# Performance work log

Hardware: AMD Instinct MI355X
Metric: run time of the kernel (lower is better)

## Reference

```python
import jax, jax.numpy as jnp
import numpy as np

N = 30000
E = 480000
F_IN = 100
HID = 64
HEADS = 4
NCLS = 47
HC = HEADS * HID  # 256
NEG_SLOPE = 0.2
BN_EPS = 1e-5


def setup_inputs() -> dict:
    key = jax.random.key(0)
    ks = jax.random.split(key, 32)
    s = 0.1
    inp = {
        'x': jax.random.normal(ks[0], (N, F_IN), jnp.float32),
        'edge_index': jax.random.randint(ks[1], (2, E), 0, N, jnp.int32),
        # layer 0: GATConv(F_IN -> HID, heads, concat=True)
        'w0': jax.random.normal(ks[2], (F_IN, HC), jnp.float32) * s,
        'as0': jax.random.normal(ks[3], (HEADS, HID), jnp.float32) * s,
        'ad0': jax.random.normal(ks[4], (HEADS, HID), jnp.float32) * s,
        'b0': jnp.zeros((HC,), jnp.float32),
        'sw0': jax.random.normal(ks[5], (F_IN, HC), jnp.float32) * s,
        'sb0': jnp.zeros((HC,), jnp.float32),
        'g0': jnp.ones((HC,), jnp.float32),
        'be0': jnp.zeros((HC,), jnp.float32),
        # layer 1: GATConv(HC -> HID, heads, concat=True)
        'w1': jax.random.normal(ks[6], (HC, HC), jnp.float32) * s,
        'as1': jax.random.normal(ks[7], (HEADS, HID), jnp.float32) * s,
        'ad1': jax.random.normal(ks[8], (HEADS, HID), jnp.float32) * s,
        'b1': jnp.zeros((HC,), jnp.float32),
        'sw1': jax.random.normal(ks[9], (HC, HC), jnp.float32) * s,
        'sb1': jnp.zeros((HC,), jnp.float32),
        'g1': jnp.ones((HC,), jnp.float32),
        'be1': jnp.zeros((HC,), jnp.float32),
        # layer 2: GATConv(HC -> NCLS, heads, concat=False)
        'w2': jax.random.normal(ks[10], (HC, HEADS * NCLS), jnp.float32) * s,
        'as2': jax.random.normal(ks[11], (HEADS, NCLS), jnp.float32) * s,
        'ad2': jax.random.normal(ks[12], (HEADS, NCLS), jnp.float32) * s,
        'b2': jnp.zeros((NCLS,), jnp.float32),
        'sw2': jax.random.normal(ks[13], (HC, NCLS), jnp.float32) * s,
        'sb2': jnp.zeros((NCLS,), jnp.float32),
    }
    return inp


def gat_conv(x, src, dst, W, a_src, a_dst, bias, heads, out_ch, concat):
    # shared linear for src/dst (PyG GATConv with int in_channels)
    h = (x @ W).reshape(N, heads, out_ch)           # [N,H,C]
    al_s = jnp.sum(h * a_src, axis=-1)              # [N,H]
    al_d = jnp.sum(h * a_dst, axis=-1)              # [N,H]
    e = jax.nn.leaky_relu(al_s[src] + al_d[dst], NEG_SLOPE)  # [E,H]
    # segment (per-destination) softmax
    m = jax.ops.segment_max(e, dst, num_segments=N)
    e = jnp.exp(e - m[dst])
    den = jax.ops.segment_sum(e, dst, num_segments=N)
    alpha = e / (den[dst] + 1e-16)                  # [E,H]
    msg = h[src] * alpha[:, :, None]                # [E,H,C]
    out = jax.ops.segment_sum(msg, dst, num_segments=N)  # [N,H,C]
    out = out.reshape(N, heads * out_ch) if concat else out.mean(axis=1)
    return out + bias


def batch_norm(x, gamma, beta):
    mu = jnp.mean(x, axis=0)
    var = jnp.var(x, axis=0)
    return gamma * (x - mu) * jax.lax.rsqrt(var + BN_EPS) + beta


def reference(x, edge_index, w0, as0, ad0, b0, sw0, sb0, g0, be0,
              w1, as1, ad1, b1, sw1, sb1, g1, be1,
              w2, as2, ad2, b2, sw2, sb2):
    src, dst = edge_index[0], edge_index[1]
    # layer 0
    h = gat_conv(x, src, dst, w0, as0, ad0, b0, HEADS, HID, True)
    h = h + x @ sw0 + sb0
    h = jax.nn.elu(batch_norm(h, g0, be0))
    # layer 1
    h2 = gat_conv(h, src, dst, w1, as1, ad1, b1, HEADS, HID, True)
    h2 = h2 + h @ sw1 + sb1
    h2 = jax.nn.elu(batch_norm(h2, g1, be1))
    # layer 2 (concat=False -> mean over heads)
    out = gat_conv(h2, src, dst, w2, as2, ad2, b2, HEADS, NCLS, False)
    out = out + h2 @ sw2 + sb2
    return jax.nn.log_softmax(out, axis=-1)
```

## Files before the change

kernel.cpp:

```cpp
#include <hip/hip_runtime.h>
#include <math.h>

#define NN 30000
#define EE 480000
#define FIN 100
#define NCLS 47
#define SCAN_B 118

typedef unsigned short ushortt;
typedef __attribute__((ext_vector_type(8))) short bf16x8;
typedef __attribute__((ext_vector_type(4))) float f32x4;
typedef __attribute__((ext_vector_type(2))) float f32x2;

__device__ unsigned char g_H8[(size_t)NN * 256];
__device__ ushortt g_Sb[(size_t)NN * 256];
__device__ float   g_S2[(size_t)NN * 48];
__device__ ushortt g_Fb[(size_t)NN * 256];
__device__ ushortt g_Xb[(size_t)NN * 128];
__device__ ushortt g_Wc0[512 * 128];
__device__ ushortt g_Wc1[512 * 256];
__device__ ushortt g_Wc2[235 * 256];
__device__ float g_als[NN * 4];
__device__ float g_ald[NN * 4];
__device__ int   g_rowptr[NN + 1];
__device__ int   g_counts[NN];
__device__ int   g_bsum[128];
__device__ int   g_esrc[EE];
__device__ float g_stat[1024];

__device__ __forceinline__ float wsum(float v) {
#pragma unroll
  for (int o = 32; o > 0; o >>= 1) v += __shfl_xor(v, o, 64);
  return v;
}
__device__ __forceinline__ float lrelu(float x) { return x > 0.f ? x : 0.2f * x; }
__device__ __forceinline__ ushortt f2bf(float f) {
  unsigned int u = __float_as_uint(f);
  unsigned int r = u + 0x7FFF + ((u >> 16) & 1);
  return (ushortt)(r >> 16);
}
__device__ __forceinline__ float bf2f(ushortt u) {
  return __uint_as_float(((unsigned int)u) << 16);
}
__device__ __forceinline__ unsigned int pk4_fp8(float f0, float f1, float f2, float f3) {
  unsigned int r = 0;
  r = __builtin_amdgcn_cvt_pk_fp8_f32(f0, f1, r, false);
  r = __builtin_amdgcn_cvt_pk_fp8_f32(f2, f3, r, true);
  return r;
}
__device__ __forceinline__ int swz(int row, int k) {
  return (k & ~63) | ((((k >> 3) & 7) ^ (row & 7)) << 3) | (k & 7);
}
__device__ __forceinline__ void glds16(const ushortt* gp, ushortt* lp) {
  __builtin_amdgcn_global_load_lds(
      (const __attribute__((address_space(1))) unsigned int*)gp,
      (__attribute__((address_space(3))) unsigned int*)lp, 16, 0, 0);
}

__global__ void count_kernel(const int* __restrict__ dst) {
  int e = blockIdx.x * blockDim.x + threadIdx.x;
  if (e < EE) atomicAdd(&g_counts[dst[e]], 1);
}
__global__ void scan1_kernel() {
  int i = blockIdx.x * 256 + threadIdx.x;
  int v = (i < NN) ? g_counts[i] : 0;
  __shared__ int sh[4];
  float fv = (float)v;
  fv = wsum(fv);
  if ((threadIdx.x & 63) == 0) sh[threadIdx.x >> 6] = (int)fv;
  __syncthreads();
  if (threadIdx.x == 0) g_bsum[blockIdx.x] = sh[0] + sh[1] + sh[2] + sh[3];
}
__global__ void scan2_kernel() {
  __shared__ int sh[128];
  int t = threadIdx.x;
  int v = (t < SCAN_B) ? g_bsum[t] : 0;
  sh[t] = v;
  __syncthreads();
  for (int off = 1; off < 128; off <<= 1) {
    int x = (t >= off) ? sh[t - off] : 0;
    __syncthreads();
    sh[t] += x;
    __syncthreads();
  }
  g_bsum[t] = sh[t] - v;
}
__global__ void scan3_kernel() {
  __shared__ int sh[256];
  int t = threadIdx.x;
  int i = blockIdx.x * 256 + t;
  int v = (i < NN) ? g_counts[i] : 0;
  sh[t] = v;
  __syncthreads();
  for (int off = 1; off < 256; off <<= 1) {
    int x = (t >= off) ? sh[t - off] : 0;
    __syncthreads();
    sh[t] += x;
    __syncthreads();
  }
  if (i < NN) {
    g_rowptr[i] = g_bsum[blockIdx.x] + sh[t] - v;
    g_counts[i] = 0;
  }
  if (i == NN - 1) g_rowptr[NN] = EE;
}
__global__ void scatter_kernel(const int* __restrict__ dst, const int* __restrict__ src) {
  int e = blockIdx.x * blockDim.x + threadIdx.x;
  if (e < EE) {
    int d = dst[e];
    int pos = g_rowptr[d] + atomicAdd(&g_counts[d], 1);
    g_esrc[pos] = src[e];
  }
}

#define CW0 (512 * 128)
#define CW1 (512 * 256)
#define CW2 (235 * 256)
__global__ void conv_kernel(const float* __restrict__ w0, const float* __restrict__ sw0,
                            const float* __restrict__ w1, const float* __restrict__ sw1,
                            const float* __restrict__ w2, const float* __restrict__ sw2,
                            const float* __restrict__ x) {
  int i = blockIdx.x * blockDim.x + threadIdx.x;
  if (i < CW0) {
    int m = i >> 7, k = i & 127;
    float v = 0.f;
    if (k < FIN) v = (m < 256) ? w0[k * 256 + m] : sw0[k * 256 + (m - 256)];
    g_Wc0[(m << 7) | swz(m, k)] = f2bf(v);
    return;
  }
  i -= CW0;
  if (i < CW1) {
    int m = i >> 8, k = i & 255;
    float v = (m < 256) ? w1[k * 256 + m] : sw1[k * 256 + (m - 256)];
    g_Wc1[(m << 8) | swz(m, k)] = f2bf(v);
    return;
  }
  i -= CW1;
  if (i < CW2) {
    int m = i >> 8, k = i & 255;
    float v = (m < 188) ? w2[(size_t)k * 188 + m] : sw2[(size_t)k * 47 + (m - 188)];
    g_Wc2[(m << 8) | swz(m, k)] = f2bf(v);
    return;
  }
  i -= CW2;
  if (i < NN * 128) {
    int r = i >> 7, k = i & 127;
    g_Xb[(r << 7) | swz(r, k)] = (k < FIN) ? f2bf(x[r * FIN + k]) : 0;
    return;
  }
  i -= NN * 128;
  if (i < NN) {
    g_counts[i] = 0;
    return;
  }
  i -= NN;
  if (i < 1024) g_stat[i] = 0.f;
}

__global__ __launch_bounds__(256) void mfma_gemm(
    const ushortt* __restrict__ A, const ushortt* __restrict__ Wt,
    unsigned char* __restrict__ out8, ushortt* __restrict__ out2b,
    float* __restrict__ out2f,
    int nrows, int Kp, int M, int S, int ld8, int ld2,
    const float* __restrict__ bias2, int pad47,
    const float* __restrict__ a_s, const float* __restrict__ a_d,
    float* __restrict__ alsp, float* __restrict__ aldp) {
  __shared__ __align__(16) ushortt smem[16896];
  ushortt* As = smem;
  ushortt* Ws = smem + 64 * 64;
  float* Ls = (float*)smem;
  int t = threadIdx.x;
  int wave = t >> 6, lane = t & 63;
  int row0 = blockIdx.y * 64, col0 = blockIdx.x * 128;
  int wr = wave >> 1, wc = wave & 1;
  int m16 = lane & 15, q = lane >> 4;
  int rin8 = lane >> 3;
  int koff = (lane & 7) * 8;

  f32x4 acc[2][4];
#pragma unroll
  for (int i = 0; i < 2; i++)
#pragma unroll
    for (int j = 0; j < 4; j++) acc[i][j] = (f32x4){0.f, 0.f, 0.f, 0.f};

  for (int k0 = 0; k0 < Kp; k0 += 64) {
#pragma unroll
    for (int r = 0; r < 2; r++) {
      int lrow = wave * 16 + r * 8;
      int ga = min(row0 + lrow + rin8, nrows - 1);
      glds16(A + (size_t)ga * Kp + k0 + koff, &As[lrow * 64]);
    }
#pragma unroll
    for (int r = 0; r < 4; r++) {
      int lrow = wave * 32 + r * 8;
      int gw = min(col0 + lrow + rin8, M - 1);
      glds16(Wt + (size_t)gw * Kp + k0 + koff, &Ws[lrow * 64]);
    }
    __syncthreads();
#pragma unroll
    for (int c = 0; c < 2; c++) {
      bf16x8 af[2], bf[4];
#pragma unroll
      for (int i = 0; i < 2; i++) {
        int row = wr * 32 + i * 16 + m16;
        int ch = (c * 4 + q) ^ (row & 7);
        af[i] = *(const bf16x8*)(&As[row * 64 + ch * 8]);
      }
#pragma unroll
      for (int i = 0; i < 4; i++) {
        int row = wc * 64 + i * 16 + m16;
        int ch = (c * 4 + q) ^ (row & 7);
        bf[i] = *(const bf16x8*)(&Ws[row * 64 + ch * 8]);
      }
#pragma unroll
      for (int rt = 0; rt < 2; rt++)
#pragma unroll
        for (int ct = 0; ct < 4; ct++)
          acc[rt][ct] = __builtin_amdgcn_mfma_f32_16x16x32_bf16(af[rt], bf[ct], acc[rt][ct], 0, 0, 0);
    }
    __syncthreads();
  }

#pragma unroll
  for (int rt = 0; rt < 2; rt++) {
#pragma unroll
    for (int ctt = 0; ctt < 4; ctt++) {
#pragma unroll
      for (int reg = 0; reg < 4; reg++) {
        int rloc = wr * 32 + rt * 16 + q * 4 + reg;
        Ls[rloc * 132 + wc * 64 + ctt * 16 + m16] = acc[rt][ctt][reg];
      }
    }
  }
  __syncthreads();
  bool all1 = (!pad47) && (col0 + 128 <= S);
  bool all2 = (col0 >= S);
  int row8 = t >> 3, seg = t & 7;
#pragma unroll
  for (int rr = 0; rr < 2; rr++) {
    int rloc = rr * 32 + row8;
    int grow = row0 + rloc;
    if (grow < nrows) {
      const float* lrow = Ls + rloc * 132 + seg * 16;
      int cbase = col0 + seg * 16;
      if (all1) {
        unsigned int q8[4];
#pragma unroll
        for (int kk = 0; kk < 4; kk++)
          q8[kk] = pk4_fp8(lrow[kk * 4], lrow[kk * 4 + 1], lrow[kk * 4 + 2], lrow[kk * 4 + 3]);
        uint4 v8 = {q8[0], q8[1], q8[2], q8[3]};
        *(uint4*)(out8 + (size_t)grow * ld8 + cbase) = v8;
        float s_p = 0.f, d_p = 0.f;
#pragma unroll
        for (int kk = 0; kk < 16; kk++) {
          s_p += lrow[kk] * a_s[cbase + kk];
          d_p += lrow[kk] * a_d[cbase + kk];
        }
        s_p += __shfl_xor(s_p, 1, 64); s_p += __shfl_xor(s_p, 2, 64);
        d_p += __shfl_xor(d_p, 1, 64); d_p += __shfl_xor(d_p, 2, 64);
        if ((seg & 3) == 0) {
          int head = cbase >> 6;
          alsp[grow * 4 + head] = s_p;
          aldp[grow * 4 + head] = d_p;
        }
      } else if (all2) {
        const float* brow = bias2 + (cbase - S);
        ushortt* orow = out2b + (size_t)grow * ld2 + (cbase - S);
        unsigned int pk[8];
#pragma unroll
        for (int kk = 0; kk < 8; kk++) {
          unsigned int lo = f2bf(lrow[kk * 2] + brow[kk * 2]);
          unsigned int hi = f2bf(lrow[kk * 2 + 1] + brow[kk * 2 + 1]);
          pk[kk] = lo | (hi << 16);
        }
        uint4 v0 = {pk[0], pk[1], pk[2], pk[3]};
        uint4 v1 = {pk[4], pk[5], pk[6], pk[7]};
        *(uint4*)(orow) = v0;
        *(uint4*)(orow + 8) = v1;
      } else {
        float pa0 = 0.f, pa1 = 0.f, pd0 = 0.f, pd1 = 0.f;
        int h0 = cbase / 47;
        for (int kk = 0; kk < 16; kk++) {
          int c = cbase + kk;
          if (c >= M) break;
          float v = lrow[kk];
          if (c < S) {
            int hd = c / 47, ch = c - hd * 47;
            int c1 = hd * 48 + ch;
            out8[(size_t)grow * ld8 + c1] =
                (unsigned char)(pk4_fp8(v, 0.f, 0.f, 0.f) & 0xFF);
            if (ch == 46) out8[(size_t)grow * ld8 + c1 + 1] = 0;
            float sw = a_s[hd * 47 + ch], dw = a_d[hd * 47 + ch];
            if (hd == h0) { pa0 += v * sw; pd0 += v * dw; }
            else { pa1 += v * sw; pd1 += v * dw; }
          } else {
            out2f[(size_t)grow * ld2 + (c - S)] = v + bias2[c - S];
          }
        }
        if (pad47 && cbase < S) {
          if (pa0 != 0.f || pd0 != 0.f) {
            atomicAdd(&alsp[grow * 4 + h0], pa0);
            atomicAdd(&aldp[grow * 4 + h0], pd0);
          }
          if ((pa1 != 0.f || pd1 != 0.f) && h0 + 1 < 4) {
            atomicAdd(&alsp[grow * 4 + h0 + 1], pa1);
            atomicAdd(&aldp[grow * 4 + h0 + 1], pd1);
          }
        }
      }
    }
  }
}

__global__ __launch_bounds__(64) void attn_kernel(const unsigned char* __restrict__ H8,
                                                  const float* __restrict__ bias,
                                                  ushortt* __restrict__ Sb) {
  __shared__ __align__(16) float p_sh[64 * 4];
  __shared__ int s_sh[64];
  int n = blockIdx.x, lane = threadIdx.x;
  int rs = g_rowptr[n], deg = g_rowptr[n + 1] - rs;
  float4 ald = *(const float4*)(g_ald + n * 4);
  int q = lane >> 4;
  float den0 = 0, den1 = 0, den2 = 0, den3 = 0;
  float a0 = 0, a1 = 0, a2 = 0, a3 = 0;
  for (int base = 0; base < deg; base += 64) {
    int j = base + lane;
    float p0 = 0, p1 = 0, p2 = 0, p3 = 0;
    int s = 0;
    if (j < deg) {
      s = g_esrc[rs + j];
      float4 av = *(const float4*)(g_als + s * 4);
      p0 = __expf(lrelu(av.x + ald.x)); den0 += p0;
      p1 = __expf(lrelu(av.y + ald.y)); den1 += p1;
      p2 = __expf(lrelu(av.z + ald.z)); den2 += p2;
      p3 = __expf(lrelu(av.w + ald.w)); den3 += p3;
    }
    p_sh[lane * 4 + 0] = p0; p_sh[lane * 4 + 1] = p1;
    p_sh[lane * 4 + 2] = p2; p_sh[lane * 4 + 3] = p3;
    s_sh[lane] = s;
    __syncthreads();
    int cnt = min(64, deg - base);
    for (int jj = 0; jj < cnt; jj++) {
      int ss = s_sh[jj];
      float p = p_sh[jj * 4 + q];
      unsigned int hv = *(const unsigned int*)(H8 + (size_t)ss * 256 + 4 * lane);
      f32x2 lo = __builtin_amdgcn_cvt_pk_f32_fp8(hv, false);
      f32x2 hi = __builtin_amdgcn_cvt_pk_f32_fp8(hv, true);
      a0 += p * lo.x;
      a1 += p * lo.y;
      a2 += p * hi.x;
      a3 += p * hi.y;
    }
    __syncthreads();
  }
  den0 = wsum(den0); den1 = wsum(den1); den2 = wsum(den2); den3 = wsum(den3);
  float denq = (q == 0) ? den0 : (q == 1) ? den1 : (q == 2) ? den2 : den3;
  float inv = 1.f / (denq + 1e-16f);
  size_t o = (size_t)n * 256 + 4 * lane;
  ushort4 sv = *(const ushort4*)(Sb + o);
  float4 bv = *(const float4*)(bias + 4 * lane);
  ushort4 ov;
  ov.x = f2bf(a0 * inv + bv.x + bf2f(sv.x));
  ov.y = f2bf(a1 * inv + bv.y + bf2f(sv.y));
  ov.z = f2bf(a2 * inv + bv.z + bf2f(sv.z));
  ov.w = f2bf(a3 * inv + bv.w + bf2f(sv.w));
  *(ushort4*)(Sb + o) = ov;
}

__global__ __launch_bounds__(64) void attn2_kernel(const unsigned char* __restrict__ H8,
                                                   const float* __restrict__ bias,
                                                   const float* __restrict__ S2,
                                                   float* __restrict__ out) {
  __shared__ __align__(16) float p_sh[64 * 4];
  __shared__ int s_sh[64];
  __shared__ float xh[4][48];
  int n = blockIdx.x, lane = threadIdx.x;
  int rs = g_rowptr[n], deg = g_rowptr[n + 1] - rs;
  float4 ald = *(const float4*)(g_ald + n * 4);
  int head = lane / 12;
  float den0 = 0, den1 = 0, den2 = 0, den3 = 0;
  float a0 = 0, a1 = 0, a2 = 0, a3 = 0;
  for (int base = 0; base < deg; base += 64) {
    int j = base + lane;
    float p0 = 0, p1 = 0, p2 = 0, p3 = 0;
    int s = 0;
    if (j < deg) {
      s = g_esrc[rs + j];
      float4 av = *(const float4*)(g_als + s * 4);
      p0 = __expf(lrelu(av.x + ald.x)); den0 += p0;
      p1 = __expf(lrelu(av.y + ald.y)); den1 += p1;
      p2 = __expf(lrelu(av.z + ald.z)); den2 += p2;
      p3 = __expf(lrelu(av.w + ald.w)); den3 += p3;
    }
    p_sh[lane * 4 + 0] = p0; p_sh[lane * 4 + 1] = p1;
    p_sh[lane * 4 + 2] = p2; p_sh[lane * 4 + 3] = p3;
    s_sh[lane] = s;
    __syncthreads();
    int cnt = min(64, deg - base);
    if (lane < 48) {
      for (int jj = 0; jj < cnt; jj++) {
        int ss = s_sh[jj];
        float p = p_sh[jj * 4 + head];
        unsigned int hv = *(const unsigned int*)(H8 + (size_t)ss * 192 + lane * 4);
        f32x2 lo = __builtin_amdgcn_cvt_pk_f32_fp8(hv, false);
        f32x2 hi = __builtin_amdgcn_cvt_pk_f32_fp8(hv, true);
        a0 += p * lo.x;
        a1 += p * lo.y;
        a2 += p * hi.x;
        a3 += p * hi.y;
      }
    }
    __syncthreads();
  }
  den0 = wsum(den0); den1 = wsum(den1); den2 = wsum(den2); den3 = wsum(den3);
  if (lane < 48) {
    float dh = (head == 0) ? den0 : (head == 1) ? den1 : (head == 2) ? den2 : den3;
    float inv = 1.f / (dh + 1e-16f);
    int chin = (lane % 12) * 4;
    xh[head][chin + 0] = a0 * inv;
    xh[head][chin + 1] = a1 * inv;
    xh[head][chin + 2] = a2 * inv;
    xh[head][chin + 3] = a3 * inv;
  }
  __syncthreads();
  float v = 0.f;
  if (lane < NCLS)
    v = 0.25f * (xh[0][lane] + xh[1][lane] + xh[2][lane] + xh[3][lane]) + bias[lane] +
        S2[(size_t)n * NCLS + lane];
  float mv = (lane < NCLS) ? v : -INFINITY;
#pragma unroll
  for (int o = 32; o > 0; o >>= 1) mv = fmaxf(mv, __shfl_xor(mv, o, 64));
  float ex = (lane < NCLS) ? __expf(v - mv) : 0.f;
  float s = wsum(ex);
  if (lane < NCLS) out[(size_t)n * NCLS + lane] = v - mv - logf(s);
}

__global__ void bn_stats_kernel(const ushortt* __restrict__ Sb, float* __restrict__ stat) {
  int c = threadIdx.x;
  int rows = (NN + gridDim.x - 1) / gridDim.x;
  int r0 = blockIdx.x * rows, r1 = min(r0 + rows, NN);
  float s = 0, q = 0;
  for (int r = r0; r < r1; r++) {
    float v = bf2f(Sb[(size_t)r * 256 + c]);
    s += v;
    q += v * v;
  }
  atomicAdd(&stat[c], s);
  atomicAdd(&stat[256 + c], q);
}
__global__ void bn_norm_kernel(const ushortt* __restrict__ Sb, const float* __restrict__ gamma,
                               const float* __restrict__ beta, const float* __restrict__ stat,
                               float* __restrict__ zs, float* __restrict__ zd) {
  int i = blockIdx.x * blockDim.x + threadIdx.x;
  if (i >= NN * 256) return;
  int c = i & 255;
  int r = i >> 8;
  float mu = stat[c] * (1.f / NN);
  float var = stat[256 + c] * (1.f / NN) - mu * mu;
  float v = (bf2f(Sb[i]) - mu) * rsqrtf(var + 1e-5f) * gamma[c] + beta[c];
  v = v > 0.f ? v : (__expf(v) - 1.f);
  g_Fb[(r << 8) | swz(r, c)] = f2bf(v);
  if (zs && i < NN * 4) {
    zs[i] = 0.f;
    zd[i] = 0.f;
  }
}

extern "C" void kernel_launch(void* const* d_in, const int* in_sizes, int n_in,
                              void* d_out, int out_size, void* d_ws, size_t ws_size,
                              hipStream_t stream) {
  const float* x = (const float*)d_in[0];
  const int* ei = (const int*)d_in[1];
  const int* src = ei;
  const int* dst = ei + EE;
  const float* w0 = (const float*)d_in[2];
  const float* as0 = (const float*)d_in[3];
  const float* ad0 = (const float*)d_in[4];
  const float* b0 = (const float*)d_in[5];
  const float* sw0 = (const float*)d_in[6];
  const float* sb0 = (const float*)d_in[7];
  const float* gm0 = (const float*)d_in[8];
  const float* be0 = (const float*)d_in[9];
  const float* w1 = (const float*)d_in[10];
  const float* as1 = (const float*)d_in[11];
  const float* ad1 = (const float*)d_in[12];
  const float* b1 = (const float*)d_in[13];
  const float* sw1 = (const float*)d_in[14];
  const float* sb1 = (const float*)d_in[15];
  const float* gm1 = (const float*)d_in[16];
  const float* be1 = (const float*)d_in[17];
  const float* w2 = (const float*)d_in[18];
  const float* as2 = (const float*)d_in[19];
  const float* ad2 = (const float*)d_in[20];
  const float* b2 = (const float*)d_in[21];
  const float* sw2 = (const float*)d_in[22];
  const float* sb2 = (const float*)d_in[23];
  float* out = (float*)d_out;

  ushortt *Sb, *Fb, *Xb, *Wc0, *Wc1, *Wc2;
  unsigned char* H8;
  float *S2, *als, *ald, *stat;
  hipGetSymbolAddress((void**)&H8, HIP_SYMBOL(g_H8));
  hipGetSymbolAddress((void**)&Sb, HIP_SYMBOL(g_Sb));
  hipGetSymbolAddress((void**)&S2, HIP_SYMBOL(g_S2));
  hipGetSymbolAddress((void**)&Fb, HIP_SYMBOL(g_Fb));
  hipGetSymbolAddress((void**)&Xb, HIP_SYMBOL(g_Xb));
  hipGetSymbolAddress((void**)&Wc0, HIP_SYMBOL(g_Wc0));
  hipGetSymbolAddress((void**)&Wc1, HIP_SYMBOL(g_Wc1));
  hipGetSymbolAddress((void**)&Wc2, HIP_SYMBOL(g_Wc2));
  hipGetSymbolAddress((void**)&als, HIP_SYMBOL(g_als));
  hipGetSymbolAddress((void**)&ald, HIP_SYMBOL(g_ald));
  hipGetSymbolAddress((void**)&stat, HIP_SYMBOL(g_stat));

  conv_kernel<<<(CW0 + CW1 + CW2 + NN * 128 + NN + 1024 + 255) / 256, 256, 0, stream>>>(
      w0, sw0, w1, sw1, w2, sw2, x);

  count_kernel<<<(EE + 255) / 256, 256, 0, stream>>>(dst);
  scan1_kernel<<<SCAN_B, 256, 0, stream>>>();
  scan2_kernel<<<1, 128, 0, stream>>>();
  scan3_kernel<<<SCAN_B, 256, 0, stream>>>();
  scatter_kernel<<<(EE + 255) / 256, 256, 0, stream>>>(dst, src);

  const int gy = (NN + 63) / 64;

  mfma_gemm<<<dim3(4, gy), 256, 0, stream>>>(Xb, Wc0, H8, Sb, nullptr, NN, 128, 512, 256,
                                             256, 256, sb0, 0, as0, ad0, als, ald);
  attn_kernel<<<NN, 64, 0, stream>>>(H8, b0, Sb);
  bn_stats_kernel<<<240, 256, 0, stream>>>(Sb, stat);
  bn_norm_kernel<<<(NN * 256 + 255) / 256, 256, 0, stream>>>(Sb, gm0, be0, stat,
                                                             nullptr, nullptr);

  mfma_gemm<<<dim3(4, gy), 256, 0, stream>>>(Fb, Wc1, H8, Sb, nullptr, NN, 256, 512, 256,
                                             256, 256, sb1, 0, as1, ad1, als, ald);
  attn_kernel<<<NN, 64, 0, stream>>>(H8, b1, Sb);
  bn_stats_kernel<<<240, 256, 0, stream>>>(Sb, stat + 512);
  bn_norm_kernel<<<(NN * 256 + 255) / 256, 256, 0, stream>>>(Sb, gm1, be1, stat + 512,
                                                             als, ald);

  mfma_gemm<<<dim3(2, gy), 256, 0, stream>>>(Fb, Wc2, H8, nullptr, S2, NN, 256, 235, 188,
                                             192, 47, sb2, 1, as2, ad2, als, ald);
  attn2_kernel<<<NN, 64, 0, stream>>>(H8, b2, S2, out);
}
```

Measured before the change: 435.9 us.

## Shrink MFMA GEMM to single-wave 32x64 tiles for more blocks

Restructures the fused GEMM from 256-thread blocks with 64x128 tiles to single-wave 64-thread blocks computing 32x64 tiles, giving four times as many blocks and a quarter of the LDS per block. The epilogue is rewritten so each lane handles half a row of 32 columns, and the attention-logit reduction is adjusted to the new head alignment. The aim is higher occupancy and better load balance on a GEMM with few column tiles. In exchange, each loaded A/W tile is reused less, so global and L2 traffic per output rises.

```diff
diff --git a/kernel.cpp b/kernel.cpp
--- a/kernel.cpp
+++ b/kernel.cpp
@@ -157,7 +157,7 @@
   if (i < 1024) g_stat[i] = 0.f;
 }
 
-__global__ __launch_bounds__(256) void mfma_gemm(
+__global__ __launch_bounds__(64) void mfma_gemm(
     const ushortt* __restrict__ A, const ushortt* __restrict__ Wt,
     unsigned char* __restrict__ out8, ushortt* __restrict__ out2b,
     float* __restrict__ out2f,
@@ -165,14 +165,12 @@
     const float* __restrict__ bias2, int pad47,
     const float* __restrict__ a_s, const float* __restrict__ a_d,
     float* __restrict__ alsp, float* __restrict__ aldp) {
-  __shared__ __align__(16) ushortt smem[16896];
+  __shared__ __align__(16) ushortt smem[(32 + 64) * 64];
   ushortt* As = smem;
-  ushortt* Ws = smem + 64 * 64;
+  ushortt* Ws = smem + 32 * 64;
   float* Ls = (float*)smem;
-  int t = threadIdx.x;
-  int wave = t >> 6, lane = t & 63;
-  int row0 = blockIdx.y * 64, col0 = blockIdx.x * 128;
-  int wr = wave >> 1, wc = wave & 1;
+  int lane = threadIdx.x;
+  int row0 = blockIdx.y * 32, col0 = blockIdx.x * 64;
   int m16 = lane & 15, q = lane >> 4;
   int rin8 = lane >> 3;
   int koff = (lane & 7) * 8;
@@ -185,16 +183,14 @@
 
   for (int k0 = 0; k0 < Kp; k0 += 64) {
 #pragma unroll
-    for (int r = 0; r < 2; r++) {
-      int lrow = wave * 16 + r * 8;
-      int ga = min(row0 + lrow + rin8, nrows - 1);
-      glds16(A + (size_t)ga * Kp + k0 + koff, &As[lrow * 64]);
-    }
-#pragma unroll
     for (int r = 0; r < 4; r++) {
-      int lrow = wave * 32 + r * 8;
-      int gw = min(col0 + lrow + rin8, M - 1);
-      glds16(Wt + (size_t)gw * Kp + k0 + koff, &Ws[lrow * 64]);
+      int ga = min(row0 + r * 8 + rin8, nrows - 1);
+      glds16(A + (size_t)ga * Kp + k0 + koff, &As[r * 8 * 64]);
+    }
+#pragma unroll
+    for (int r = 0; r < 8; r++) {
+      int gw = min(col0 + r * 8 + rin8, M - 1);
+      glds16(Wt + (size_t)gw * Kp + k0 + koff, &Ws[r * 8 * 64]);
     }
     __syncthreads();
 #pragma unroll
@@ -202,13 +198,13 @@
       bf16x8 af[2], bf[4];
 #pragma unroll
       for (int i = 0; i < 2; i++) {
-        int row = wr * 32 + i * 16 + m16;
+        int row = i * 16 + m16;
         int ch = (c * 4 + q) ^ (row & 7);
         af[i] = *(const bf16x8*)(&As[row * 64 + ch * 8]);
       }
 #pragma unroll
       for (int i = 0; i < 4; i++) {
-        int row = wc * 64 + i * 16 + m16;
+        int row = i * 16 + m16;
         int ch = (c * 4 + q) ^ (row & 7);
         bf[i] = *(const bf16x8*)(&Ws[row * 64 + ch * 8]);
       }
@@ -227,85 +223,92 @@
     for (int ctt = 0; ctt < 4; ctt++) {
 #pragma unroll
       for (int reg = 0; reg < 4; reg++) {
-        int rloc = wr * 32 + rt * 16 + q * 4 + reg;
-        Ls[rloc * 132 + wc * 64 + ctt * 16 + m16] = acc[rt][ctt][reg];
+        int rloc = rt * 16 + q * 4 + reg;
+        Ls[rloc * 68 + ctt * 16 + m16] = acc[rt][ctt][reg];
       }
     }
   }
   __syncthreads();
-  bool all1 = (!pad47) && (col0 + 128 <= S);
-  bool all2 = (col0 >= S);
-  int row8 = t >> 3, seg = t & 7;
-#pragma unroll
-  for (int rr = 0; rr < 2; rr++) {
-    int rloc = rr * 32 + row8;
-    int grow = row0 + rloc;
-    if (grow < nrows) {
-      const float* lrow = Ls + rloc * 132 + seg * 16;
-      int cbase = col0 + seg * 16;
-      if (all1) {
-        unsigned int q8[4];
-#pragma unroll
-        for (int kk = 0; kk < 4; kk++)
-          q8[kk] = pk4_fp8(lrow[kk * 4], lrow[kk * 4 + 1], lrow[kk * 4 + 2], lrow[kk * 4 + 3]);
-        uint4 v8 = {q8[0], q8[1], q8[2], q8[3]};
-        *(uint4*)(out8 + (size_t)grow * ld8 + cbase) = v8;
-        float s_p = 0.f, d_p = 0.f;
+  int rloc = lane >> 1, half = lane & 1;
+  int grow = row0 + rloc;
+  if (grow < nrows) {
+    const float* lrow = Ls + rloc * 68 + half * 32;
+    int cbase = col0 + half * 32;
+    bool all1 = (!pad47) && (col0 + 64 <= S);
+    bool all2 = (col0 >= S);
+    if (all1) {
+      unsigned int q8[8];
+#pragma unroll
+      for (int kk = 0; kk < 8; kk++)
+        q8[kk] = pk4_fp8(lrow[kk * 4], lrow[kk * 4 + 1], lrow[kk * 4 + 2], lrow[kk * 4 + 3]);
+      uint4 v0 = {q8[0], q8[1], q8[2], q8[3]};
+      uint4 v1 = {q8[4], q8[5], q8[6], q8[7]};
+      *(uint4*)(out8 + (size_t)grow * ld8 + cbase) = v0;
+      *(uint4*)(out8 + (size_t)grow * ld8 + cbase + 16) = v1;
+      float s_p = 0.f, d_p = 0.f;
+#pragma unroll
+      for (int kk = 0; kk < 32; kk++) {
+        s_p += lrow[kk] * a_s[cbase + kk];
+        d_p += lrow[kk] * a_d[cbase + kk];
+      }
+      s_p += __shfl_xor(s_p, 1, 64);
+      d_p += __shfl_xor(d_p, 1, 64);
+      if (half == 0) {
+        int head = col0 >> 6;
+        alsp[grow * 4 + head] = s_p;
+        aldp[grow * 4 + head] = d_p;
+      }
+    } else if (all2) {
+      const float* brow = bias2 + (cbase - S);
+      if (out2b) {
+        ushortt* orow = out2b + (size_t)grow * ld2 + (cbase - S);
+        unsigned int pk[16];
 #pragma unroll
         for (int kk = 0; kk < 16; kk++) {
-          s_p += lrow[kk] * a_s[cbase + kk];
-          d_p += lrow[kk] * a_d[cbase + kk];
-        }
-        s_p += __shfl_xor(s_p, 1, 64); s_p += __shfl_xor(s_p, 2, 64);
-        d_p += __shfl_xor(d_p, 1, 64); d_p += __shfl_xor(d_p, 2, 64);
-        if ((seg & 3) == 0) {
-          int head = cbase >> 6;
-          alsp[grow * 4 + head] = s_p;
-          aldp[grow * 4 + head] = d_p;
-        }
-      } else if (all2) {
-        const float* brow = bias2 + (cbase - S);
-        ushortt* orow = out2b + (size_t)grow * ld2 + (cbase - S);
-        unsigned int pk[8];
-#pragma unroll
-        for (int kk = 0; kk < 8; kk++) {
           unsigned int lo = f2bf(lrow[kk * 2] + brow[kk * 2]);
           unsigned int hi = f2bf(lrow[kk * 2 + 1] + brow[kk * 2 + 1]);
           pk[kk] = lo | (hi << 16);
         }
-        uint4 v0 = {pk[0], pk[1], pk[2], pk[3]};
-        uint4 v1 = {pk[4], pk[5], pk[6], pk[7]};
-        *(uint4*)(orow) = v0;
-        *(uint4*)(orow + 8) = v1;
+#pragma unroll
+        for (int v = 0; v < 4; v++) {
+          uint4 u = {pk[v * 4], pk[v * 4 + 1], pk[v * 4 + 2], pk[v * 4 + 3]};
+          *(uint4*)(orow + v * 8) = u;
+        }
       } else {
-        float pa0 = 0.f, pa1 = 0.f, pd0 = 0.f, pd1 = 0.f;
-        int h0 = cbase / 47;
-        for (int kk = 0; kk < 16; kk++) {
+        for (int kk = 0; kk < 32; kk++) {
           int c = cbase + kk;
           if (c >= M) break;
-          float v = lrow[kk];
-          if (c < S) {
-            int hd = c / 47, ch = c - hd * 47;
-            int c1 = hd * 48 + ch;
-            out8[(size_t)grow * ld8 + c1] =
-                (unsigned char)(pk4_fp8(v, 0.f, 0.f, 0.f) & 0xFF);
-            if (ch == 46) out8[(size_t)grow * ld8 + c1 + 1] = 0;
-            float sw = a_s[hd * 47 + ch], dw = a_d[hd * 47 + ch];
-            if (hd == h0) { pa0 += v * sw; pd0 += v * dw; }
-            else { pa1 += v * sw; pd1 += v * dw; }
-          } else {
-            out2f[(size_t)grow * ld2 + (c - S)] = v + bias2[c - S];
-          }
+          out2f[(size_t)grow * ld2 + (c - S)] = lrow[kk] + brow[kk];
         }
-        if (pad47 && cbase < S) {
-          if (pa0 != 0.f || pd0 != 0.f) {
-            atomicAdd(&alsp[grow * 4 + h0], pa0);
-            atomicAdd(&aldp[grow * 4 + h0], pd0);
-          }
-          if ((pa1 != 0.f || pd1 != 0.f) && h0 + 1 < 4) {
-            atomicAdd(&alsp[grow * 4 + h0 + 1], pa1);
-            atomicAdd(&aldp[grow * 4 + h0 + 1], pd1);
-          }
+      }
+    } else {
+      float pa0 = 0.f, pa1 = 0.f, pd0 = 0.f, pd1 = 0.f;
+      int h0 = cbase / 47;
+      for (int kk = 0; kk < 32; kk++) {
+        int c = cbase + kk;
+        if (c >= M) break;
+        float v = lrow[kk];
+        if (c < S) {
+          int hd = c / 47, ch = c - hd * 47;
+          int c1 = hd * 48 + ch;
+          out8[(size_t)grow * ld8 + c1] =
+              (unsigned char)(pk4_fp8(v, 0.f, 0.f, 0.f) & 0xFF);
+          if (ch == 46) out8[(size_t)grow * ld8 + c1 + 1] = 0;
+          float sw = a_s[hd * 47 + ch], dw = a_d[hd * 47 + ch];
+          if (hd == h0) { pa0 += v * sw; pd0 += v * dw; }
+          else { pa1 += v * sw; pd1 += v * dw; }
+        } else {
+          out2f[(size_t)grow * ld2 + (c - S)] = v + bias2[c - S];
+        }
+      }
+      if (pad47 && cbase < S) {
+        if (pa0 != 0.f || pd0 != 0.f) {
+          atomicAdd(&alsp[grow * 4 + h0], pa0);
+          atomicAdd(&aldp[grow * 4 + h0], pd0);
+        }
+        if ((pa1 != 0.f || pd1 != 0.f) && h0 + 1 < 4) {
+          atomicAdd(&alsp[grow * 4 + h0 + 1], pa1);
+          atomicAdd(&aldp[grow * 4 + h0 + 1], pd1);
         }
       }
     }
@@ -521,23 +524,23 @@
   scan3_kernel<<<SCAN_B, 256, 0, stream>>>();
   scatter_kernel<<<(EE + 255) / 256, 256, 0, stream>>>(dst, src);
 
-  const int gy = (NN + 63) / 64;
-
-  mfma_gemm<<<dim3(4, gy), 256, 0, stream>>>(Xb, Wc0, H8, Sb, nullptr, NN, 128, 512, 256,
-                                             256, 256, sb0, 0, as0, ad0, als, ald);
+  const int gy = (NN + 31) / 32;
+
+  mfma_gemm<<<dim3(8, gy), 64, 0, stream>>>(Xb, Wc0, H8, Sb, nullptr, NN, 128, 512, 256,
+                                            256, 256, sb0, 0, as0, ad0, als, ald);
   attn_kernel<<<NN, 64, 0, stream>>>(H8, b0, Sb);
   bn_stats_kernel<<<240, 256, 0, stream>>>(Sb, stat);
   bn_norm_kernel<<<(NN * 256 + 255) / 256, 256, 0, stream>>>(Sb, gm0, be0, stat,
                                                              nullptr, nullptr);
 
-  mfma_gemm<<<dim3(4, gy), 256, 0, stream>>>(Fb, Wc1, H8, Sb, nullptr, NN, 256, 512, 256,
-                                             256, 256, sb1, 0, as1, ad1, als, ald);
+  mfma_gemm<<<dim3(8, gy), 64, 0, stream>>>(Fb, Wc1, H8, Sb, nullptr, NN, 256, 512, 256,
+                                            256, 256, sb1, 0, as1, ad1, als, ald);
   attn_kernel<<<NN, 64, 0, stream>>>(H8, b1, Sb);
   bn_stats_kernel<<<240, 256, 0, stream>>>(Sb, stat + 512);
   bn_norm_kernel<<<(NN * 256 + 255) / 256, 256, 0, stream>>>(Sb, gm1, be1, stat + 512,
                                                              als, ald);
 
-  mfma_gemm<<<dim3(2, gy), 256, 0, stream>>>(Fb, Wc2, H8, nullptr, S2, NN, 256, 235, 188,
-                                             192, 47, sb2, 1, as2, ad2, als, ald);
+  mfma_gemm<<<dim3(4, gy), 64, 0, stream>>>(Fb, Wc2, H8, nullptr, S2, NN, 256, 235, 188,
+                                            192, 47, sb2, 1, as2, ad2, als, ald);
   attn2_kernel<<<NN, 64, 0, stream>>>(H8, b2, S2, out);
 }
```

Result: slower. 488.7 us (+12.1%).
